# Performance work log

Measured on AMD Instinct MI355X. Metric: run time of the kernel, lower is better.

## Reference

```python
import jax, jax.numpy as jnp
import numpy as np

N_NODES = 100000
D_IN = 128
D_OUT = 128
SHAPES = {"r1": 1, "r2": 2, "r3": 3}
N_EDGES = {"r1": 400000, "r2": 300000, "r3": 200000}


def setup_inputs() -> dict:
    key = jax.random.key(0)
    ks = jax.random.split(key, 10)
    inp = {
        "x": jax.random.normal(ks[0], (N_NODES, D_IN), dtype=jnp.float32),
        "A_r1": jax.random.normal(ks[1], (D_IN * 1, D_OUT), dtype=jnp.float32) * 0.05,
        "A_r2": jax.random.normal(ks[2], (D_IN * 2, D_OUT), dtype=jnp.float32) * 0.05,
        "A_r3": jax.random.normal(ks[3], (D_IN * 3, D_OUT), dtype=jnp.float32) * 0.05,
        "C_w": jax.random.normal(ks[4], (D_IN, D_OUT), dtype=jnp.float32) * 0.05,
        "C_b": jax.random.normal(ks[5], (D_OUT,), dtype=jnp.float32) * 0.05,
    }
    for j, (name, shape) in enumerate(SHAPES.items()):
        n = N_EDGES[name] * shape
        inp[f"ei_{name}"] = jax.random.randint(ks[6 + j], (2, n), 0, N_NODES, dtype=jnp.int64)
    return inp


def _edge_type_agg(x, edge_indices, A, shape):
    # edge_indices: [2, n_edges*shape]; row0 = sources, row1 reshaped -> dest per hyperedge
    dest = edge_indices[1].reshape(-1, shape)[:, 0]          # [n_edges]
    gathered = x[edge_indices[0]].reshape(-1, shape * x.shape[1])  # [n_edges, shape*D_IN]
    msg = gathered @ A                                        # [n_edges, D_OUT]
    # 1/count(dest) normalization (torch.unique counts == per-type in-degree)
    deg = jax.ops.segment_sum(jnp.ones_like(dest, dtype=msg.dtype), dest, num_segments=x.shape[0])
    msg = msg / deg[dest][:, None]
    return jax.ops.segment_sum(msg, dest, num_segments=x.shape[0])  # scatter_add


def reference(x, ei_r1, ei_r2, ei_r3, A_r1, A_r2, A_r3, C_w, C_b):
    agg = (_edge_type_agg(x, ei_r1, A_r1, 1)
           + _edge_type_agg(x, ei_r2, A_r2, 2)
           + _edge_type_agg(x, ei_r3, A_r3, 3))
    return x @ C_w + C_b + agg
```

## Files before the change

### kernel.cpp

```cpp
#include <hip/hip_runtime.h>

#define N_NODES 100000
#define D 128

typedef unsigned short u16;
typedef short s16x8 __attribute__((ext_vector_type(8)));
typedef float f32x4 __attribute__((ext_vector_type(4)));


#define ENTS_OFF 2804224L
#define AT_OFF   9204224L
#define G_OFF    9433600L

__device__ __forceinline__ u16 f2b(float f) {
    union { float f; unsigned u; } v; v.f = f;
    unsigned r = (v.u + 0x7FFFu + ((v.u >> 16) & 1u)) >> 16;
    return (u16)r;
}
__device__ __forceinline__ unsigned pk(float lo, float hi) {
    return (unsigned)f2b(lo) | ((unsigned)f2b(hi) << 16);
}
__device__ __forceinline__ float blo(unsigned w) { return __uint_as_float(w << 16); }
__device__ __forceinline__ float bhi(unsigned w) { return __uint_as_float(w & 0xFFFF0000u); }


__global__ __launch_bounds__(256) void init_kernel(
    const float* __restrict__ x,
    const float* __restrict__ A1, const float* __restrict__ A2,
    const float* __restrict__ A3, const float* __restrict__ Cw,
    u16* __restrict__ ATb, u16* __restrict__ G, int* __restrict__ deg) {
    int b = blockIdx.x, t = threadIdx.x;
    if (b < 293) {
        int i0 = (b * 256 + t) * 4;
#pragma unroll
        for (int r = 0; r < 4; r++)
            if (i0 + r < 300000) deg[i0 + r] = 0;
        return;
    }
    if (b < 741) {
        int mb = b - 293;
        int m = mb >> 6;
        int idx = (mb & 63) * 256 + t;
        int n = idx >> 7, kk = idx & 127;
        const float* src; int srow;
        if (m == 0)      { src = A1; srow = kk; }
        else if (m < 3)  { src = A2; srow = (m - 1) * 128 + kk; }
        else if (m < 6)  { src = A3; srow = (m - 3) * 128 + kk; }
        else             { src = Cw; srow = kk; }
        ATb[m * 16384 + n * 128 + kk] = f2b(src[(long)srow * 128 + n]);
        return;
    }
    int f = (b - 741) * 256 + t;
    int node = f >> 4, j = f & 15;
    const float* xr = x + (long)node * 128 + j * 8;
    float4 v0 = *(const float4*)xr;
    float4 v1 = *(const float4*)(xr + 4);
    uint4 o;
    o.x = pk(v0.x, v0.y); o.y = pk(v0.z, v0.w);
    o.z = pk(v1.x, v1.y); o.w = pk(v1.z, v1.w);
    *(uint4*)(G + (long)node * 896 + 768 + j * 8) = o;
}


__global__ __launch_bounds__(256) void deg_all(
    const int* __restrict__ e1, const int* __restrict__ e2, const int* __restrict__ e3,
    int ne1, int ne2, int ne3, int* __restrict__ deg) {
    int g = blockIdx.x * 256 + threadIdx.x;
    if (g < ne1) {
        atomicAdd(&deg[e1[ne1 + g]], 1);
    } else if (g < ne1 + ne2) {
        int e = g - ne1;
        atomicAdd(&deg[N_NODES + e2[ne2 * 2 + e * 2]], 1);
    } else if (g < ne1 + ne2 + ne3) {
        int e = g - ne1 - ne2;
        atomicAdd(&deg[2 * N_NODES + e3[ne3 * 3 + e * 3]], 1);
    }
}

__device__ __forceinline__ int ucnt(const int* deg, int d) {
    return deg[d] + 2 * deg[N_NODES + d] + 3 * deg[2 * N_NODES + d];
}


__global__ __launch_bounds__(256) void scan_reduce_u(const int* __restrict__ deg,
                                                     int* __restrict__ bsums, int n) {
    __shared__ int s[256];
    int t = threadIdx.x;
    int base = blockIdx.x * 1024 + t * 4;
    int loc = 0;
#pragma unroll
    for (int r = 0; r < 4; r++) {
        int idx = base + r;
        if (idx < n) loc += ucnt(deg, idx);
    }
    s[t] = loc;
    for (int off = 128; off > 0; off >>= 1) {
        __syncthreads();
        if (t < off) s[t] += s[t + off];
    }
    if (t == 0) bsums[blockIdx.x] = s[0];
}

__global__ __launch_bounds__(512) void scan_tops(const int* __restrict__ bsums,
                                                 int* __restrict__ boffs,
                                                 int* __restrict__ offs, int nb, int n) {
    __shared__ int s[512];
    int t = threadIdx.x;
    int v = (t < nb) ? bsums[t] : 0;
    s[t] = v;
    for (int off = 1; off < 512; off <<= 1) {
        __syncthreads();
        int x = (t >= off) ? s[t - off] : 0;
        __syncthreads();
        s[t] += x;
    }
    if (t < nb) boffs[t] = s[t] - v;
    if (t == nb - 1) offs[n] = s[t];
}

__global__ __launch_bounds__(256) void scan_final_u(
    const int* __restrict__ deg, const int* __restrict__ boffs,
    int* __restrict__ offs, int* __restrict__ cursor, int n) {
    __shared__ int s[256];
    int t = threadIdx.x;
    int base = blockIdx.x * 1024 + t * 4;
    int v[4], p[4];
#pragma unroll
    for (int r = 0; r < 4; r++) {
        int idx = base + r;
        v[r] = (idx < n) ? ucnt(deg, idx) : 0;
    }
    p[0] = 0; p[1] = v[0]; p[2] = v[0] + v[1]; p[3] = v[0] + v[1] + v[2];
    int tsum = p[3] + v[3];
    s[t] = tsum;
    for (int off = 1; off < 256; off <<= 1) {
        __syncthreads();
        int x = (t >= off) ? s[t - off] : 0;
        __syncthreads();
        s[t] += x;
    }
    int texcl = s[t] - tsum + boffs[blockIdx.x];
#pragma unroll
    for (int r = 0; r < 4; r++) {
        int idx = base + r;
        if (idx < n) {
            int val = texcl + p[r];
            offs[idx] = val;
            int c1 = deg[idx], c2 = deg[N_NODES + idx];
            cursor[idx] = val;
            cursor[N_NODES + idx] = val + c1;
            cursor[2 * N_NODES + idx] = val + c1 + 2 * c2;
        }
    }
}


__global__ __launch_bounds__(256) void scatter_all(
    const int* __restrict__ e1, const int* __restrict__ e2, const int* __restrict__ e3,
    int ne1, int ne2, int ne3, const int* __restrict__ deg,
    int* __restrict__ cursor, int* __restrict__ ents) {
    int g = blockIdx.x * 256 + threadIdx.x;
    if (g < ne1) {
        int dest = e1[ne1 + g];
        int pos = atomicAdd(&cursor[dest], 1);
        ents[pos] = e1[g];
    } else if (g < ne1 + ne2) {
        int e = g - ne1;
        int dest = e2[ne2 * 2 + e * 2];
        int c2 = deg[N_NODES + dest];
        int pos = atomicAdd(&cursor[N_NODES + dest], 1);
        ents[pos]      = e2[e * 2];
        ents[pos + c2] = e2[e * 2 + 1];
    } else if (g < ne1 + ne2 + ne3) {
        int e = g - ne1 - ne2;
        int dest = e3[ne3 * 3 + e * 3];
        int c3 = deg[2 * N_NODES + dest];
        int pos = atomicAdd(&cursor[2 * N_NODES + dest], 1);
        ents[pos]          = e3[e * 3];
        ents[pos + c3]     = e3[e * 3 + 1];
        ents[pos + 2 * c3] = e3[e * 3 + 2];
    }
}


__global__ __launch_bounds__(256) void agg_all(
    u16* __restrict__ G, const int* __restrict__ ents,
    const int* __restrict__ offs, const int* __restrict__ deg) {
    const int lane = threadIdx.x & 63;
    const int wv = threadIdx.x >> 6;
    int wid = blockIdx.x * 4 + wv;
    const int nw = gridDim.x * 4;
    const int col = lane * 2;

    for (int d = wid; d < N_NODES; d += nw) {
        const int lo = offs[d];
        const int c1 = deg[d], c2 = deg[N_NODES + d], c3 = deg[2 * N_NODES + d];
        float a0l = 0, a0h = 0, a1l = 0, a1h = 0, a2l = 0, a2h = 0;
        float a3l = 0, a3h = 0, a4l = 0, a4h = 0, a5l = 0, a5h = 0;

        for (int p = 0; p < c1; p += 4) {
            unsigned w[4]; float m[4];
#pragma unroll
            for (int i = 0; i < 4; i++) {
                int q = (p + i < c1) ? p + i : c1 - 1;
                int src = ents[lo + q];
                w[i] = *(const unsigned*)(G + (long)src * 896 + 768 + col);
                m[i] = (p + i < c1) ? 1.0f : 0.0f;
            }
#pragma unroll
            for (int i = 0; i < 4; i++) {
                a0l = fmaf(m[i], blo(w[i]), a0l);
                a0h = fmaf(m[i], bhi(w[i]), a0h);
            }
        }
        const int o1 = lo + c1;
        for (int p = 0; p < c2; p += 4) {
            unsigned wa[4], wb[4]; float m[4];
#pragma unroll
            for (int i = 0; i < 4; i++) {
                int q = (p + i < c2) ? p + i : c2 - 1;
                int sa = ents[o1 + q];
                int sb = ents[o1 + q + c2];
                wa[i] = *(const unsigned*)(G + (long)sa * 896 + 768 + col);
                wb[i] = *(const unsigned*)(G + (long)sb * 896 + 768 + col);
                m[i] = (p + i < c2) ? 1.0f : 0.0f;
            }
#pragma unroll
            for (int i = 0; i < 4; i++) {
                a1l = fmaf(m[i], blo(wa[i]), a1l); a1h = fmaf(m[i], bhi(wa[i]), a1h);
                a2l = fmaf(m[i], blo(wb[i]), a2l); a2h = fmaf(m[i], bhi(wb[i]), a2h);
            }
        }
        const int o3 = o1 + 2 * c2;
        for (int p = 0; p < c3; p += 4) {
            unsigned wa[4], wb[4], wc[4]; float m[4];
#pragma unroll
            for (int i = 0; i < 4; i++) {
                int q = (p + i < c3) ? p + i : c3 - 1;
                int sa = ents[o3 + q];
                int sb = ents[o3 + q + c3];
                int sc = ents[o3 + q + 2 * c3];
                wa[i] = *(const unsigned*)(G + (long)sa * 896 + 768 + col);
                wb[i] = *(const unsigned*)(G + (long)sb * 896 + 768 + col);
                wc[i] = *(const unsigned*)(G + (long)sc * 896 + 768 + col);
                m[i] = (p + i < c3) ? 1.0f : 0.0f;
            }
#pragma unroll
            for (int i = 0; i < 4; i++) {
                a3l = fmaf(m[i], blo(wa[i]), a3l); a3h = fmaf(m[i], bhi(wa[i]), a3h);
                a4l = fmaf(m[i], blo(wb[i]), a4l); a4h = fmaf(m[i], bhi(wb[i]), a4h);
                a5l = fmaf(m[i], blo(wc[i]), a5l); a5h = fmaf(m[i], bhi(wc[i]), a5h);
            }
        }
        const float i1 = c1 ? 1.0f / (float)c1 : 0.0f;
        const float i2 = c2 ? 1.0f / (float)c2 : 0.0f;
        const float i3 = c3 ? 1.0f / (float)c3 : 0.0f;
        u16* gd = G + (long)d * 896 + col;
        *(unsigned*)(gd)       = pk(a0l * i1, a0h * i1);
        *(unsigned*)(gd + 128) = pk(a1l * i2, a1h * i2);
        *(unsigned*)(gd + 256) = pk(a2l * i2, a2h * i2);
        *(unsigned*)(gd + 384) = pk(a3l * i3, a3h * i3);
        *(unsigned*)(gd + 512) = pk(a4l * i3, a4h * i3);
        *(unsigned*)(gd + 640) = pk(a5l * i3, a5h * i3);
    }
}


__global__ __launch_bounds__(256) void gemm_out(
    const u16* __restrict__ G, const u16* __restrict__ AT,
    const float* __restrict__ Cb, float* __restrict__ out) {
    __shared__ __align__(16) float smemf[64 * 132];
    typedef u16 XsT[64][40];
    XsT* Xs = reinterpret_cast<XsT*>(smemf);

    const int t = threadIdx.x;
    const int d0 = blockIdx.x * 64;
    const int lane = t & 63, wv = t >> 6;
    const int nbase = wv * 32, quad = lane >> 4, lrow = lane & 15;

    f32x4 acc[4][2];
#pragma unroll
    for (int mi = 0; mi < 4; mi++)
#pragma unroll
        for (int ni = 0; ni < 2; ni++) acc[mi][ni] = (f32x4)(0.0f);

    for (int s = 0; s < 7; s++) {
#pragma unroll
        for (int i = 0; i < 4; i++) {
            int f = i * 256 + t;
            int row = f >> 4, k8 = f & 15;
            long rs = (d0 + row < N_NODES) ? d0 + row : N_NODES - 1;
            uint4 v = *(const uint4*)(G + rs * 896 + s * 128 + k8 * 8);
            *(uint4*)&Xs[k8 >> 2][row][(k8 & 3) * 8] = v;
        }
        __syncthreads();
        const u16* B = AT + s * 16384;
        s16x8 bfrag[2][4];
#pragma unroll
        for (int ni = 0; ni < 2; ni++)
#pragma unroll
            for (int c = 0; c < 4; c++)
                bfrag[ni][c] = *(const s16x8*)(B + (nbase + ni * 16 + lrow) * 128 +
                                               c * 32 + quad * 8);
        s16x8 afrag[4][4];
#pragma unroll
        for (int mi = 0; mi < 4; mi++)
#pragma unroll
            for (int c = 0; c < 4; c++)
                afrag[mi][c] = *(const s16x8*)&Xs[c][mi * 16 + lrow][quad * 8];
#pragma unroll
        for (int c = 0; c < 4; c++)
#pragma unroll
            for (int mi = 0; mi < 4; mi++)
#pragma unroll
                for (int ni = 0; ni < 2; ni++)
                    acc[mi][ni] = __builtin_amdgcn_mfma_f32_16x16x32_bf16(
                        afrag[mi][c], bfrag[ni][c], acc[mi][ni], 0, 0, 0);
        __syncthreads();
    }

#pragma unroll
    for (int mi = 0; mi < 4; mi++)
#pragma unroll
        for (int ni = 0; ni < 2; ni++)
#pragma unroll
            for (int reg = 0; reg < 4; reg++) {
                int row = mi * 16 + quad * 4 + reg;
                int colq = nbase + ni * 16 + lrow;
                smemf[row * 132 + colq] = acc[mi][ni][reg];
            }
    __syncthreads();
#pragma unroll
    for (int i = 0; i < 8; i++) {
        int f = i * 256 + t;
        int row = f >> 5;
        int colq = (f & 31) * 4;
        if (d0 + row < N_NODES) {
            float4 v = *(const float4*)&smemf[row * 132 + colq];
            float4 b = *(const float4*)&Cb[colq];
            v.x += b.x; v.y += b.y; v.z += b.z; v.w += b.w;
            *(float4*)&out[(long)(d0 + row) * 128 + colq] = v;
        }
    }
}


extern "C" void kernel_launch(void* const* d_in, const int* in_sizes, int n_in,
                              void* d_out, int out_size, void* d_ws, size_t ws_size,
                              hipStream_t stream) {
    const float* x  = (const float*)d_in[0];
    const float* A1 = (const float*)d_in[1];
    const float* A2 = (const float*)d_in[2];
    const float* A3 = (const float*)d_in[3];
    const float* Cw = (const float*)d_in[4];
    const float* Cb = (const float*)d_in[5];
    const int* e1 = (const int*)d_in[6];
    const int* e2 = (const int*)d_in[7];
    const int* e3 = (const int*)d_in[8];
    float* out = (float*)d_out;

    int* ws = (int*)d_ws;
    int* deg    = ws;
    int* offs   = ws + 300000;
    int* cursor = ws + 400001;
    int* bsums  = ws + 700001;
    int* boffs  = ws + 700513;
    int* ents   = (int*)((char*)d_ws + ENTS_OFF);
    u16* ATb    = (u16*)((char*)d_ws + AT_OFF);
    u16* G      = (u16*)((char*)d_ws + G_OFF);

    const int NE1 = in_sizes[6] / 2;
    const int NE2 = in_sizes[7] / (2 * 2);
    const int NE3 = in_sizes[8] / (2 * 3);
    const int NET = NE1 + NE2 + NE3;
    const int n = N_NODES;
    const int NB = (n + 1023) / 1024;

    init_kernel<<<293 + 448 + 6250, 256, 0, stream>>>(x, A1, A2, A3, Cw, ATb, G, deg);
    deg_all<<<(NET + 255) / 256, 256, 0, stream>>>(e1, e2, e3, NE1, NE2, NE3, deg);
    scan_reduce_u<<<NB, 256, 0, stream>>>(deg, bsums, n);
    scan_tops<<<1, 512, 0, stream>>>(bsums, boffs, offs, NB, n);
    scan_final_u<<<NB, 256, 0, stream>>>(deg, boffs, offs, cursor, n);
    scatter_all<<<(NET + 255) / 256, 256, 0, stream>>>(e1, e2, e3, NE1, NE2, NE3,
                                                       deg, cursor, ents);
    agg_all<<<2048, 256, 0, stream>>>(G, ents, offs, deg);
    gemm_out<<<(N_NODES + 63) / 64, 256, 0, stream>>>(G, ATb, Cb, out);
}
```

Measured before the change: 364.5 us.

## Fuse neighbor aggregation into the GEMM kernel, dropping the wide G buffer

Merges the gather-and-average aggregation with the bf16 MFMA output GEMM in one kernel. Each 64-node block aggregates its six slot segments directly into shared memory and feeds them to the MFMAs, with a compact 128-wide bf16 x buffer replacing the 896-wide G intermediate. This removes the write and reread of the aggregated features and one launch. In exchange, the aggregation now runs one wave per 16 rows serially inside the GEMM block, with a sync per slot, which may lower memory-level parallelism and add load imbalance.

```diff
diff --git a/kernel.cpp b/kernel.cpp
--- a/kernel.cpp
+++ b/kernel.cpp
@@ -10,7 +10,7 @@
 
 #define ENTS_OFF 2804224L
 #define AT_OFF   9204224L
-#define G_OFF    9433600L
+#define XB_OFF   9433600L
 
 __device__ __forceinline__ u16 f2b(float f) {
     union { float f; unsigned u; } v; v.f = f;
@@ -28,7 +28,7 @@
     const float* __restrict__ x,
     const float* __restrict__ A1, const float* __restrict__ A2,
     const float* __restrict__ A3, const float* __restrict__ Cw,
-    u16* __restrict__ ATb, u16* __restrict__ G, int* __restrict__ deg) {
+    u16* __restrict__ ATb, u16* __restrict__ xb, int* __restrict__ deg) {
     int b = blockIdx.x, t = threadIdx.x;
     if (b < 293) {
         int i0 = (b * 256 + t) * 4;
@@ -58,7 +58,7 @@
     uint4 o;
     o.x = pk(v0.x, v0.y); o.y = pk(v0.z, v0.w);
     o.z = pk(v1.x, v1.y); o.w = pk(v1.z, v1.w);
-    *(uint4*)(G + (long)node * 896 + 768 + j * 8) = o;
+    *(uint4*)(xb + (long)node * 128 + j * 8) = o;
 }
 
 
@@ -183,100 +183,25 @@
 }
 
 
-__global__ __launch_bounds__(256) void agg_all(
-    u16* __restrict__ G, const int* __restrict__ ents,
-    const int* __restrict__ offs, const int* __restrict__ deg) {
-    const int lane = threadIdx.x & 63;
-    const int wv = threadIdx.x >> 6;
-    int wid = blockIdx.x * 4 + wv;
-    const int nw = gridDim.x * 4;
-    const int col = lane * 2;
-
-    for (int d = wid; d < N_NODES; d += nw) {
-        const int lo = offs[d];
-        const int c1 = deg[d], c2 = deg[N_NODES + d], c3 = deg[2 * N_NODES + d];
-        float a0l = 0, a0h = 0, a1l = 0, a1h = 0, a2l = 0, a2h = 0;
-        float a3l = 0, a3h = 0, a4l = 0, a4h = 0, a5l = 0, a5h = 0;
-
-        for (int p = 0; p < c1; p += 4) {
-            unsigned w[4]; float m[4];
-#pragma unroll
-            for (int i = 0; i < 4; i++) {
-                int q = (p + i < c1) ? p + i : c1 - 1;
-                int src = ents[lo + q];
-                w[i] = *(const unsigned*)(G + (long)src * 896 + 768 + col);
-                m[i] = (p + i < c1) ? 1.0f : 0.0f;
-            }
-#pragma unroll
-            for (int i = 0; i < 4; i++) {
-                a0l = fmaf(m[i], blo(w[i]), a0l);
-                a0h = fmaf(m[i], bhi(w[i]), a0h);
-            }
-        }
-        const int o1 = lo + c1;
-        for (int p = 0; p < c2; p += 4) {
-            unsigned wa[4], wb[4]; float m[4];
-#pragma unroll
-            for (int i = 0; i < 4; i++) {
-                int q = (p + i < c2) ? p + i : c2 - 1;
-                int sa = ents[o1 + q];
-                int sb = ents[o1 + q + c2];
-                wa[i] = *(const unsigned*)(G + (long)sa * 896 + 768 + col);
-                wb[i] = *(const unsigned*)(G + (long)sb * 896 + 768 + col);
-                m[i] = (p + i < c2) ? 1.0f : 0.0f;
-            }
-#pragma unroll
-            for (int i = 0; i < 4; i++) {
-                a1l = fmaf(m[i], blo(wa[i]), a1l); a1h = fmaf(m[i], bhi(wa[i]), a1h);
-                a2l = fmaf(m[i], blo(wb[i]), a2l); a2h = fmaf(m[i], bhi(wb[i]), a2h);
-            }
-        }
-        const int o3 = o1 + 2 * c2;
-        for (int p = 0; p < c3; p += 4) {
-            unsigned wa[4], wb[4], wc[4]; float m[4];
-#pragma unroll
-            for (int i = 0; i < 4; i++) {
-                int q = (p + i < c3) ? p + i : c3 - 1;
-                int sa = ents[o3 + q];
-                int sb = ents[o3 + q + c3];
-                int sc = ents[o3 + q + 2 * c3];
-                wa[i] = *(const unsigned*)(G + (long)sa * 896 + 768 + col);
-                wb[i] = *(const unsigned*)(G + (long)sb * 896 + 768 + col);
-                wc[i] = *(const unsigned*)(G + (long)sc * 896 + 768 + col);
-                m[i] = (p + i < c3) ? 1.0f : 0.0f;
-            }
-#pragma unroll
-            for (int i = 0; i < 4; i++) {
-                a3l = fmaf(m[i], blo(wa[i]), a3l); a3h = fmaf(m[i], bhi(wa[i]), a3h);
-                a4l = fmaf(m[i], blo(wb[i]), a4l); a4h = fmaf(m[i], bhi(wb[i]), a4h);
-                a5l = fmaf(m[i], blo(wc[i]), a5l); a5h = fmaf(m[i], bhi(wc[i]), a5h);
-            }
-        }
-        const float i1 = c1 ? 1.0f / (float)c1 : 0.0f;
-        const float i2 = c2 ? 1.0f / (float)c2 : 0.0f;
-        const float i3 = c3 ? 1.0f / (float)c3 : 0.0f;
-        u16* gd = G + (long)d * 896 + col;
-        *(unsigned*)(gd)       = pk(a0l * i1, a0h * i1);
-        *(unsigned*)(gd + 128) = pk(a1l * i2, a1h * i2);
-        *(unsigned*)(gd + 256) = pk(a2l * i2, a2h * i2);
-        *(unsigned*)(gd + 384) = pk(a3l * i3, a3h * i3);
-        *(unsigned*)(gd + 512) = pk(a4l * i3, a4h * i3);
-        *(unsigned*)(gd + 640) = pk(a5l * i3, a5h * i3);
-    }
-}
-
-
-__global__ __launch_bounds__(256) void gemm_out(
-    const u16* __restrict__ G, const u16* __restrict__ AT,
-    const float* __restrict__ Cb, float* __restrict__ out) {
-    __shared__ __align__(16) float smemf[64 * 132];
-    typedef u16 XsT[64][40];
-    XsT* Xs = reinterpret_cast<XsT*>(smemf);
+__global__ __launch_bounds__(256) void agg_gemm(
+    const u16* __restrict__ xb, const int* __restrict__ ents,
+    const int* __restrict__ offs, const int* __restrict__ deg,
+    const u16* __restrict__ AT, const float* __restrict__ Cb,
+    float* __restrict__ out) {
+    __shared__ __align__(16) u16 Xs[4][64][40];
+    __shared__ int4 meta[64];
 
     const int t = threadIdx.x;
     const int d0 = blockIdx.x * 64;
     const int lane = t & 63, wv = t >> 6;
     const int nbase = wv * 32, quad = lane >> 4, lrow = lane & 15;
+    const int col = lane * 2;
+
+    if (t < 64) {
+        int dd = (d0 + t < N_NODES) ? d0 + t : N_NODES - 1;
+        meta[t] = make_int4(offs[dd], deg[dd], deg[N_NODES + dd], deg[2 * N_NODES + dd]);
+    }
+    __syncthreads();
 
     f32x4 acc[4][2];
 #pragma unroll
@@ -284,62 +209,89 @@
 #pragma unroll
         for (int ni = 0; ni < 2; ni++) acc[mi][ni] = (f32x4)(0.0f);
 
+#pragma unroll
     for (int s = 0; s < 7; s++) {
+        if (s < 6) {
+            for (int j = 0; j < 16; j++) {
+                int row = wv * 16 + j;
+                int4 m = meta[row];
+                int cnt = (s == 0) ? m.y : (s < 3) ? m.z : m.w;
+                int base = m.x + (s >= 1 ? m.y : 0) + (s >= 2 ? m.z : 0) +
+                           (s >= 3 ? m.z : 0) + (s >= 4 ? m.w : 0) + (s >= 5 ? m.w : 0);
+                float al = 0.0f, ah = 0.0f;
+                for (int p = 0; p < cnt; p += 4) {
+                    unsigned w[4];
+#pragma unroll
+                    for (int i = 0; i < 4; i++) {
+                        int q = (p + i < cnt) ? p + i : cnt - 1;
+                        int src = ents[base + q];
+                        unsigned v = *(const unsigned*)(xb + (long)src * 128 + col);
+                        w[i] = (p + i < cnt) ? v : 0u;
+                    }
+#pragma unroll
+                    for (int i = 0; i < 4; i++) { al += blo(w[i]); ah += bhi(w[i]); }
+                }
+                float inv = cnt ? 1.0f / (float)cnt : 0.0f;
+                *(unsigned*)&Xs[col >> 5][row][col & 31] = pk(al * inv, ah * inv);
+            }
+        } else {
+#pragma unroll
+            for (int i = 0; i < 4; i++) {
+                int f = i * 256 + t;
+                int row = f >> 4, k8 = f & 15;
+                long rs = (d0 + row < N_NODES) ? d0 + row : N_NODES - 1;
+                uint4 v = *(const uint4*)(xb + rs * 128 + k8 * 8);
+                *(uint4*)&Xs[k8 >> 2][row][(k8 & 3) * 8] = v;
+            }
+        }
+        __syncthreads();
+        const u16* B = AT + s * 16384;
+#pragma unroll
+        for (int c = 0; c < 4; c++) {
+            s16x8 a[4], b2[2];
+#pragma unroll
+            for (int mi = 0; mi < 4; mi++)
+                a[mi] = *(const s16x8*)&Xs[c][mi * 16 + lrow][quad * 8];
+#pragma unroll
+            for (int ni = 0; ni < 2; ni++)
+                b2[ni] = *(const s16x8*)(B + (nbase + ni * 16 + lrow) * 128 +
+                                         c * 32 + quad * 8);
+#pragma unroll
+            for (int mi = 0; mi < 4; mi++)
+#pragma unroll
+                for (int ni = 0; ni < 2; ni++)
+                    acc[mi][ni] = __builtin_amdgcn_mfma_f32_16x16x32_bf16(
+                        a[mi], b2[ni], acc[mi][ni], 0, 0, 0);
+        }
+        __syncthreads();
+    }
+
+    float* smf = (float*)&Xs[0][0][0];
+#pragma unroll
+    for (int h = 0; h < 2; h++) {
+        if (h) __syncthreads();
+#pragma unroll
+        for (int mi = 2 * h; mi < 2 * h + 2; mi++)
+#pragma unroll
+            for (int ni = 0; ni < 2; ni++)
+#pragma unroll
+                for (int reg = 0; reg < 4; reg++) {
+                    int row = (mi - 2 * h) * 16 + quad * 4 + reg;
+                    int cq = nbase + ni * 16 + lrow;
+                    smf[row * 132 + cq] = acc[mi][ni][reg];
+                }
+        __syncthreads();
 #pragma unroll
         for (int i = 0; i < 4; i++) {
             int f = i * 256 + t;
-            int row = f >> 4, k8 = f & 15;
-            long rs = (d0 + row < N_NODES) ? d0 + row : N_NODES - 1;
-            uint4 v = *(const uint4*)(G + rs * 896 + s * 128 + k8 * 8);
-            *(uint4*)&Xs[k8 >> 2][row][(k8 & 3) * 8] = v;
-        }
-        __syncthreads();
-        const u16* B = AT + s * 16384;
-        s16x8 bfrag[2][4];
-#pragma unroll
-        for (int ni = 0; ni < 2; ni++)
-#pragma unroll
-            for (int c = 0; c < 4; c++)
-                bfrag[ni][c] = *(const s16x8*)(B + (nbase + ni * 16 + lrow) * 128 +
-                                               c * 32 + quad * 8);
-        s16x8 afrag[4][4];
-#pragma unroll
-        for (int mi = 0; mi < 4; mi++)
-#pragma unroll
-            for (int c = 0; c < 4; c++)
-                afrag[mi][c] = *(const s16x8*)&Xs[c][mi * 16 + lrow][quad * 8];
-#pragma unroll
-        for (int c = 0; c < 4; c++)
-#pragma unroll
-            for (int mi = 0; mi < 4; mi++)
-#pragma unroll
-                for (int ni = 0; ni < 2; ni++)
-                    acc[mi][ni] = __builtin_amdgcn_mfma_f32_16x16x32_bf16(
-                        afrag[mi][c], bfrag[ni][c], acc[mi][ni], 0, 0, 0);
-        __syncthreads();
-    }
-
-#pragma unroll
-    for (int mi = 0; mi < 4; mi++)
-#pragma unroll
-        for (int ni = 0; ni < 2; ni++)
-#pragma unroll
-            for (int reg = 0; reg < 4; reg++) {
-                int row = mi * 16 + quad * 4 + reg;
-                int colq = nbase + ni * 16 + lrow;
-                smemf[row * 132 + colq] = acc[mi][ni][reg];
+            int row = f >> 5, cq = (f & 31) * 4;
+            int gr = d0 + h * 32 + row;
+            if (gr < N_NODES) {
+                float4 v = *(const float4*)&smf[row * 132 + cq];
+                float4 b = *(const float4*)&Cb[cq];
+                v.x += b.x; v.y += b.y; v.z += b.z; v.w += b.w;
+                *(float4*)&out[(long)gr * 128 + cq] = v;
             }
-    __syncthreads();
-#pragma unroll
-    for (int i = 0; i < 8; i++) {
-        int f = i * 256 + t;
-        int row = f >> 5;
-        int colq = (f & 31) * 4;
-        if (d0 + row < N_NODES) {
-            float4 v = *(const float4*)&smemf[row * 132 + colq];
-            float4 b = *(const float4*)&Cb[colq];
-            v.x += b.x; v.y += b.y; v.z += b.z; v.w += b.w;
-            *(float4*)&out[(long)(d0 + row) * 128 + colq] = v;
         }
     }
 }
@@ -367,7 +319,7 @@
     int* boffs  = ws + 700513;
     int* ents   = (int*)((char*)d_ws + ENTS_OFF);
     u16* ATb    = (u16*)((char*)d_ws + AT_OFF);
-    u16* G      = (u16*)((char*)d_ws + G_OFF);
+    u16* xb     = (u16*)((char*)d_ws + XB_OFF);
 
     const int NE1 = in_sizes[6] / 2;
     const int NE2 = in_sizes[7] / (2 * 2);
@@ -376,13 +328,12 @@
     const int n = N_NODES;
     const int NB = (n + 1023) / 1024;
 
-    init_kernel<<<293 + 448 + 6250, 256, 0, stream>>>(x, A1, A2, A3, Cw, ATb, G, deg);
+    init_kernel<<<293 + 448 + 6250, 256, 0, stream>>>(x, A1, A2, A3, Cw, ATb, xb, deg);
     deg_all<<<(NET + 255) / 256, 256, 0, stream>>>(e1, e2, e3, NE1, NE2, NE3, deg);
     scan_reduce_u<<<NB, 256, 0, stream>>>(deg, bsums, n);
     scan_tops<<<1, 512, 0, stream>>>(bsums, boffs, offs, NB, n);
     scan_final_u<<<NB, 256, 0, stream>>>(deg, boffs, offs, cursor, n);
     scatter_all<<<(NET + 255) / 256, 256, 0, stream>>>(e1, e2, e3, NE1, NE2, NE3,
                                                        deg, cursor, ents);
-    agg_all<<<2048, 256, 0, stream>>>(G, ents, offs, deg);
-    gemm_out<<<(N_NODES + 63) / 64, 256, 0, stream>>>(G, ATb, Cb, out);
-}
+    agg_gemm<<<(N_NODES + 63) / 64, 256, 0, stream>>>(xb, ents, offs, deg, ATb, Cb, out);
+}
```

New measurement: 435.0 us. +19.3%, slower.
